# Kernel optimization log

Measured on AMD Instinct MI355X. Metric: run time of the kernel, lower is better.

The kernel has to match this reference:

```python
import jax, jax.numpy as jnp
import numpy as np

D_MODEL = 1024
NUM_HEADS = 16
WINDOW = 256
HEAD_DIM = D_MODEL // NUM_HEADS


def setup_inputs() -> dict:
    key = jax.random.key(0)
    ks = jax.random.split(key, 5)
    B, L, D = 2, 2048, D_MODEL
    s = 1.0 / np.sqrt(D)
    x = jax.random.normal(ks[0], (B, L, D), dtype=jnp.float32)
    w_qkv = jax.random.normal(ks[1], (3 * D, D), dtype=jnp.float32) * s
    b_qkv = jnp.zeros((3 * D,), dtype=jnp.float32)
    w_proj = jax.random.normal(ks[2], (D, D), dtype=jnp.float32) * s
    b_proj = jnp.zeros((D,), dtype=jnp.float32)
    return {"x": x, "w_qkv": w_qkv, "b_qkv": b_qkv, "w_proj": w_proj, "b_proj": b_proj}


def reference(x, w_qkv, b_qkv, w_proj, b_proj):
    B, L, D = x.shape
    H, E = NUM_HEADS, HEAD_DIM
    scale = 1.0 / jnp.sqrt(jnp.asarray(E, dtype=x.dtype))
    # torch Linear: y = x @ W.T + b
    qkv = (x @ w_qkv.T + b_qkv).reshape(B, L, 3, H, E)
    qkv = jnp.transpose(qkv, (2, 0, 3, 1, 4))  # [3, B, H, L, E]
    q, k, v = qkv[0], qkv[1], qkv[2]
    scores = jnp.einsum('bhle,bhme->bhlm', q, k) * scale  # [B,H,L,L]
    i = jnp.arange(L)[:, None]
    j = jnp.arange(L)[None, :]
    mask = (j > i) | ((i - j) >= WINDOW)  # causal OR outside window
    scores = jnp.where(mask, jnp.asarray(-10000.0, dtype=scores.dtype), scores)
    attn = jax.nn.softmax(scores, axis=-1)
    out = jnp.einsum('bhlm,bhme->bhle', attn, v)  # [B,H,L,E]
    out = jnp.transpose(out, (0, 2, 1, 3)).reshape(B, L, D)
    return out @ w_proj.T + b_proj
```

## Files before the change

### kernel.cpp

```cpp
#include <hip/hip_runtime.h>

typedef __bf16 bf16x8 __attribute__((ext_vector_type(8)));
typedef float f32x4 __attribute__((ext_vector_type(4)));
typedef unsigned short u16;
typedef unsigned int u32;

__device__ __forceinline__ u16 f2bf(float f) {
  u32 u = __builtin_bit_cast(u32, f);
  u32 r = (u + 0x7FFFu + ((u >> 16) & 1u)) >> 16;
  return (u16)r;
}

__device__ __forceinline__ void gload16(const u16* g, u16* lds_base) {
  __builtin_amdgcn_global_load_lds(
      (const __attribute__((address_space(1))) void*)g,
      (__attribute__((address_space(3))) void*)lds_base, 16, 0, 0);
}

__global__ void cast_all(const float* __restrict__ x,  u16* __restrict__ xo,
                         const float* __restrict__ wq, u16* __restrict__ wqo,
                         const float* __restrict__ wp, u16* __restrict__ wpo) {
  const int NX = (2 * 2048 * 1024) / 4;
  const int NQ = (3072 * 1024) / 4;
  const int NP = (1024 * 1024) / 4;
  int i = blockIdx.x * blockDim.x + threadIdx.x;
  int stride = gridDim.x * blockDim.x;
  for (; i < NX + NQ + NP; i += stride) {
    const float4* s; uint2* d; int j;
    if (i < NX)            { s = (const float4*)x;  d = (uint2*)xo;  j = i; }
    else if (i < NX + NQ)  { s = (const float4*)wq; d = (uint2*)wqo; j = i - NX; }
    else                   { s = (const float4*)wp; d = (uint2*)wpo; j = i - NX - NQ; }
    float4 f = s[j];
    uint2 o;
    o.x = (u32)f2bf(f.x) | ((u32)f2bf(f.y) << 16);
    o.y = (u32)f2bf(f.z) | ((u32)f2bf(f.w) << 16);
    d[j] = o;
  }
}

template<int OUT_BF16, int BM, int BN>
__global__ __launch_bounds__(256) void gemm_nt(
    const u16* __restrict__ A, const u16* __restrict__ W,
    const float* __restrict__ bias, void* __restrict__ Cout,
    int M, int N, int K)
{
  constexpr int MT = BM / 32;
  constexpr int NT = BN / 32;
  __shared__ u16 Alds[2][BM][32];
  __shared__ u16 Blds[2][BN][32];
  const int tid  = threadIdx.x;
  const int lane = tid & 63;
  const int wave = tid >> 6;
  const int wm = (wave >> 1) * (BM / 2);
  const int wn = (wave & 1) * (BN / 2);

  const int b    = blockIdx.x;
  const int xcd  = b & 7;
  const int slot = b >> 3;
  const int npx  = (N / BN) >> 3;
  const int m0 = (slot / npx) * BM;
  const int n0 = (xcd * npx + slot % npx) * BN;

  const int quad = lane >> 4;
  const int li   = lane & 15;

  const u16* ga = &A[(size_t)(m0 + wave * (BM / 4) + (lane >> 2)) * K + (lane & 3) * 8];
  const u16* gb = &W[(size_t)(n0 + wave * (BN / 4) + (lane >> 2)) * K + (lane & 3) * 8];

  auto stage = [&](int buf, int k0) {
#pragma unroll
    for (int i = 0; i < BM / 64; i++)
      gload16(ga + (size_t)i * 16 * K + k0, &Alds[buf][wave * (BM / 4) + i * 16][0]);
#pragma unroll
    for (int i = 0; i < BN / 64; i++)
      gload16(gb + (size_t)i * 16 * K + k0, &Blds[buf][wave * (BN / 4) + i * 16][0]);
  };

  f32x4 acc[MT][NT] = {};
  const int niter = K / 32;

  stage(0, 0);

#pragma unroll 2
  for (int kt = 0; kt < niter; kt++) {
    __syncthreads();
    if (kt + 1 < niter) stage((kt + 1) & 1, (kt + 1) * 32);
    const int buf = kt & 1;
    bf16x8 af[MT], bfr[NT];
#pragma unroll
    for (int t = 0; t < MT; t++)
      af[t] = *(const bf16x8*)&Alds[buf][wm + t * 16 + li][quad * 8];
#pragma unroll
    for (int t = 0; t < NT; t++)
      bfr[t] = *(const bf16x8*)&Blds[buf][wn + t * 16 + li][quad * 8];
#pragma unroll
    for (int mt = 0; mt < MT; mt++)
#pragma unroll
      for (int nt = 0; nt < NT; nt++)
        acc[mt][nt] = __builtin_amdgcn_mfma_f32_16x16x32_bf16(af[mt], bfr[nt], acc[mt][nt], 0, 0, 0);
  }

#pragma unroll
  for (int mt = 0; mt < MT; mt++)
#pragma unroll
    for (int nt = 0; nt < NT; nt++) {
      int gn = n0 + wn + nt * 16 + li;
      float bv = bias[gn];
#pragma unroll
      for (int r = 0; r < 4; r++) {
        int gm = m0 + wm + mt * 16 + quad * 4 + r;
        float v = acc[mt][nt][r] + bv;
        if (OUT_BF16)
          ((u16*)Cout)[(size_t)gm * N + gn] = f2bf(v);
        else
          ((float*)Cout)[(size_t)gm * N + gn] = v;
      }
    }
}

__global__ __launch_bounds__(256, 4) void attn_kernel(const u16* __restrict__ qkv,
                                                      u16* __restrict__ aout)
{
  const int L = 2048, DQ = 3072, D = 1024;
  const int bid  = blockIdx.x;
  const int wgid = (bid & 7) * 128 + (bid >> 3);
  const int qt = wgid & 31;
  const int h  = (wgid >> 5) & 15;
  const int b  = wgid >> 9;
  const int q0 = qt * 64;
  const int tid  = threadIdx.x;
  const int lane = tid & 63;
  const int wave = tid >> 6;
  const int quad = lane >> 4;
  const int li   = lane & 15;

  __shared__ u16 Klds[64][68];
  __shared__ u16 Vt[64][68];
  __shared__ u16 Plds[4][16][68];

  const u16* base = qkv + (size_t)b * L * DQ + h * 64;

  bf16x8 qf[2];
  {
    const u16* qsrc = base + (size_t)(q0 + wave * 16 + li) * DQ;
    qf[0] = *(const bf16x8*)&qsrc[quad * 8];
    qf[1] = *(const bf16x8*)&qsrc[32 + quad * 8];
  }

  f32x4 O[4] = {};
  float lsum[4] = {0.f, 0.f, 0.f, 0.f};

  const float scale = 0.125f;
  const int gq = q0 + wave * 16 + quad * 4;

  const int sr2 = (tid >> 3) * 2, sc = (tid & 7) * 8;
  const u16* ksbase = base + D;
  const u16* vsbase = base + 2 * D;
  uint4 kr0, kr1, vr0, vr1;
  auto loadkv = [&](int t) {
    int kb = q0 - 256 + t * 64;
    const u16* ks = ksbase + (size_t)kb * DQ;
    const u16* vs = vsbase + (size_t)kb * DQ;
    kr0 = *(const uint4*)&ks[(size_t)sr2 * DQ + sc];
    kr1 = *(const uint4*)&ks[(size_t)(sr2 + 1) * DQ + sc];
    vr0 = *(const uint4*)&vs[(size_t)sr2 * DQ + sc];
    vr1 = *(const uint4*)&vs[(size_t)(sr2 + 1) * DQ + sc];
  };

  const int t0 = (qt < 4) ? (4 - qt) : 0;
  loadkv(t0);

  for (int t = t0; t < 5; t++) {
    const int kb = q0 - 256 + t * 64;
    __syncthreads();
    *(uint4*)&Klds[sr2][sc]     = kr0;
    *(uint4*)&Klds[sr2 + 1][sc] = kr1;
    {
      u32 a0[4] = {vr0.x, vr0.y, vr0.z, vr0.w};
      u32 a1[4] = {vr1.x, vr1.y, vr1.z, vr1.w};
#pragma unroll
      for (int j2 = 0; j2 < 4; j2++) {
        u32 lo0 = a0[j2] & 0xffffu, hi0 = a0[j2] >> 16;
        u32 lo1 = a1[j2] & 0xffffu, hi1 = a1[j2] >> 16;
        *(u32*)&Vt[sc + 2 * j2][sr2]     = lo0 | (lo1 << 16);
        *(u32*)&Vt[sc + 2 * j2 + 1][sr2] = hi0 | (hi1 << 16);
      }
    }
    __syncthreads();
    if (t + 1 < 5) loadkv(t + 1);

    f32x4 sacc[4] = {};
#pragma unroll
    for (int nt = 0; nt < 4; nt++) {
      bf16x8 kf0 = *(const bf16x8*)&Klds[nt * 16 + li][quad * 8];
      bf16x8 kf1 = *(const bf16x8*)&Klds[nt * 16 + li][32 + quad * 8];
      sacc[nt] = __builtin_amdgcn_mfma_f32_16x16x32_bf16(qf[0], kf0, sacc[nt], 0, 0, 0);
      sacc[nt] = __builtin_amdgcn_mfma_f32_16x16x32_bf16(qf[1], kf1, sacc[nt], 0, 0, 0);
    }

#pragma unroll
    for (int nt = 0; nt < 4; nt++) {
      int gj = kb + nt * 16 + li;
#pragma unroll
      for (int r = 0; r < 4; r++) {
        bool masked = (gj > gq + r) || ((gq + r) - gj >= 256);
        float p = masked ? 0.f : __expf(sacc[nt][r] * scale - 12.f);
        lsum[r] += p;
        Plds[wave][quad * 4 + r][nt * 16 + li] = f2bf(p);
      }
    }

    bf16x8 pf0 = *(const bf16x8*)&Plds[wave][li][quad * 8];
    bf16x8 pf1 = *(const bf16x8*)&Plds[wave][li][32 + quad * 8];
#pragma unroll
    for (int nt = 0; nt < 4; nt++) {
      bf16x8 vb0 = *(const bf16x8*)&Vt[nt * 16 + li][quad * 8];
      bf16x8 vb1 = *(const bf16x8*)&Vt[nt * 16 + li][32 + quad * 8];
      O[nt] = __builtin_amdgcn_mfma_f32_16x16x32_bf16(pf0, vb0, O[nt], 0, 0, 0);
      O[nt] = __builtin_amdgcn_mfma_f32_16x16x32_bf16(pf1, vb1, O[nt], 0, 0, 0);
    }
  }

#pragma unroll
  for (int d = 1; d < 16; d <<= 1)
#pragma unroll
    for (int r = 0; r < 4; r++)
      lsum[r] += __shfl_xor(lsum[r], d, 64);
#pragma unroll
  for (int r = 0; r < 4; r++) {
    float inv = 1.f / lsum[r];
#pragma unroll
    for (int nt = 0; nt < 4; nt++)
      aout[(size_t)(b * L + gq + r) * D + h * 64 + nt * 16 + li] = f2bf(O[nt][r] * inv);
  }
}

extern "C" void kernel_launch(void* const* d_in, const int* in_sizes, int n_in,
                              void* d_out, int out_size, void* d_ws, size_t ws_size,
                              hipStream_t stream) {
  const float* x      = (const float*)d_in[0];
  const float* w_qkv  = (const float*)d_in[1];
  const float* b_qkv  = (const float*)d_in[2];
  const float* w_proj = (const float*)d_in[3];
  const float* b_proj = (const float*)d_in[4];
  float* out = (float*)d_out;

  char* ws = (char*)d_ws;
  u16* x_bf     = (u16*)(ws);
  u16* wqkv_bf  = (u16*)(ws + ((size_t)8  << 20));
  u16* wproj_bf = (u16*)(ws + ((size_t)14 << 20));
  u16* qkv_bf   = (u16*)(ws + ((size_t)16 << 20));
  u16* attn_bf  = (u16*)(ws + ((size_t)40 << 20));

  cast_all<<<1024, 256, 0, stream>>>(x, x_bf, w_qkv, wqkv_bf, w_proj, wproj_bf);

  gemm_nt<1, 128, 128><<<(4096 / 128) * (3072 / 128), 256, 0, stream>>>(
      x_bf, wqkv_bf, b_qkv, qkv_bf, 4096, 3072, 1024);

  attn_kernel<<<1024, 256, 0, stream>>>(qkv_bf, attn_bf);

  gemm_nt<0, 128, 128><<<(4096 / 128) * (1024 / 128), 256, 0, stream>>>(
      attn_bf, wproj_bf, b_proj, out, 4096, 1024, 1024);
}
```

Measured before the change: 157.6 us.

## Use K=64 tiled GEMM with XOR-swizzled LDS for output projection

Adds a specialized 128x128 GEMM for the output projection that stages 64-wide K slices per iteration instead of 32. It XOR-swizzles the LDS column blocks to avoid bank conflicts on the fragment reads. This halves the number of barrier and stage rounds per K loop. In exchange it doubles the LDS footprint to 64 KB, which may reduce occupancy.

```diff
diff --git a/kernel.cpp b/kernel.cpp
--- a/kernel.cpp
+++ b/kernel.cpp
@@ -118,6 +118,85 @@
     }
 }
 
+__global__ __launch_bounds__(256) void gemm_nt64(
+    const u16* __restrict__ A, const u16* __restrict__ W,
+    const float* __restrict__ bias, float* __restrict__ Cout,
+    int M, int N, int K)
+{
+  __shared__ u16 Alds[2][128][64];
+  __shared__ u16 Blds[2][128][64];
+  const int tid  = threadIdx.x;
+  const int lane = tid & 63;
+  const int wave = tid >> 6;
+  const int wm = (wave >> 1) * 64;
+  const int wn = (wave & 1) * 64;
+
+  const int b    = blockIdx.x;
+  const int xcd  = b & 7;
+  const int slot = b >> 3;
+  const int npx  = (N / 128) >> 3;
+  const int m0 = (slot / npx) * 128;
+  const int n0 = (xcd * npx + slot % npx) * 128;
+
+  const int quad = lane >> 4;
+  const int li   = lane & 15;
+
+  const int r8 = lane >> 3;
+  const int db = (lane & 7) ^ r8;
+  const u16* ga = A + (size_t)(m0 + wave * 32 + r8) * K + db * 8;
+  const u16* gb = W + (size_t)(n0 + wave * 32 + r8) * K + db * 8;
+
+  auto stage = [&](int buf, int k0) {
+#pragma unroll
+    for (int i = 0; i < 4; i++)
+      gload16(ga + (size_t)(i * 8) * K + k0, &Alds[buf][wave * 32 + i * 8][0]);
+#pragma unroll
+    for (int i = 0; i < 4; i++)
+      gload16(gb + (size_t)(i * 8) * K + k0, &Blds[buf][wave * 32 + i * 8][0]);
+  };
+
+  f32x4 acc[4][4] = {};
+  const int niter = K / 64;
+
+  stage(0, 0);
+
+  for (int kt = 0; kt < niter; kt++) {
+    __syncthreads();
+    if (kt + 1 < niter) stage((kt + 1) & 1, (kt + 1) * 64);
+    const int buf = kt & 1;
+    bf16x8 af[4][2], bfr[4][2];
+#pragma unroll
+    for (int t = 0; t < 4; t++)
+#pragma unroll
+      for (int k = 0; k < 2; k++) {
+        const int pos = ((k * 4 + quad) ^ (li & 7)) * 8;
+        af[t][k]  = *(const bf16x8*)&Alds[buf][wm + t * 16 + li][pos];
+        bfr[t][k] = *(const bf16x8*)&Blds[buf][wn + t * 16 + li][pos];
+      }
+#pragma unroll
+    for (int mt = 0; mt < 4; mt++)
+#pragma unroll
+      for (int nt = 0; nt < 4; nt++)
+#pragma unroll
+        for (int k = 0; k < 2; k++)
+          acc[mt][nt] = __builtin_amdgcn_mfma_f32_16x16x32_bf16(
+              af[mt][k], bfr[nt][k], acc[mt][nt], 0, 0, 0);
+  }
+
+#pragma unroll
+  for (int mt = 0; mt < 4; mt++)
+#pragma unroll
+    for (int nt = 0; nt < 4; nt++) {
+      int gn = n0 + wn + nt * 16 + li;
+      float bv = bias[gn];
+#pragma unroll
+      for (int r = 0; r < 4; r++) {
+        int gm = m0 + wm + mt * 16 + quad * 4 + r;
+        Cout[(size_t)gm * N + gn] = acc[mt][nt][r] + bv;
+      }
+    }
+}
+
 __global__ __launch_bounds__(256, 4) void attn_kernel(const u16* __restrict__ qkv,
                                                       u16* __restrict__ aout)
 {
@@ -259,6 +338,6 @@
 
   attn_kernel<<<1024, 256, 0, stream>>>(qkv_bf, attn_bf);
 
-  gemm_nt<0, 128, 128><<<(4096 / 128) * (1024 / 128), 256, 0, stream>>>(
+  gemm_nt64<<<(4096 / 128) * (1024 / 128), 256, 0, stream>>>(
       attn_bf, wproj_bf, b_proj, out, 4096, 1024, 1024);
 }
```

Result: no change. 157.4 us (-0.1%).
